# Kernel tuning notes

Hardware: AMD Instinct MI355X
Metric: run time of the kernel (lower is better)

The kernel has to match this reference:

```python
import jax, jax.numpy as jnp
import numpy as np
from jax import lax

N, C, H, W = 5, 256, 128, 128
RATIO = 16
KS = 3
SIGMA = 1.0
THRE = 0.01


def _conv2d_same(x, w):
    k = w.shape[-1]
    p = (k - 1) // 2
    return lax.conv_general_dilated(x, w, (1, 1), [(p, p), (p, p)],
                                    dimension_numbers=('NCHW', 'OIHW', 'NCHW'))


def _gaussian2d():
    c = KS // 2
    x, y = np.mgrid[-c:KS - c, -c:KS - c]
    g = 1.0 / (2.0 * np.pi * SIGMA) * np.exp(-(x ** 2 + y ** 2) / (2.0 * SIGMA ** 2))
    return jnp.asarray(g, jnp.float32).reshape(1, 1, KS, KS)


def _gaussian1d():
    x = np.arange(-(KS - 1) // 2, (KS + 1) // 2, dtype=np.float32)
    g = np.exp(-x ** 2 / (2.0 * SIGMA ** 2))
    g = g / g.sum()
    return jnp.asarray(g, jnp.float32).reshape(1, 1, KS)


def setup_inputs() -> dict:
    key = jax.random.key(0)
    ks = jax.random.split(key, 12)
    s = 0.05
    return {
        'feat': jax.random.normal(ks[0], (N, C, H, W), jnp.float32),
        'mlp_w1': jax.random.normal(ks[1], (C // RATIO, C), jnp.float32) * s,
        'mlp_w2': jax.random.normal(ks[2], (C, C // RATIO), jnp.float32) * s,
        'sp_req_w': jax.random.normal(ks[3], (1, 2, 3, 3), jnp.float32) * s,
        'ch_fus_w': jax.random.normal(ks[4], (C, 2 * C), jnp.float32) * s,
        'sp_fus_w': jax.random.normal(ks[5], (1, 2), jnp.float32) * s,
        'st_w1': jax.random.normal(ks[6], (4 * C, 2 * C), jnp.float32) * s,
        'st_b1': jax.random.normal(ks[7], (4 * C,), jnp.float32) * s,
        'st_w2': jax.random.normal(ks[8], (4 * C, 4 * C), jnp.float32) * s,
        'st_b2': jax.random.normal(ks[9], (4 * C,), jnp.float32) * s,
        'st_w3': jax.random.normal(ks[10], (1, 4 * C), jnp.float32) * s,
        'st_b3': jax.random.normal(ks[11], (1,), jnp.float32) * s,
    }


def _forward(feat, mlp_w1, mlp_w2, sp_req_w, ch_fus_w, sp_fus_w,
             st_w1, st_b1, st_w2, st_b2, st_w3, st_b3):
    g2 = _gaussian2d()
    g1 = _gaussian1d()

    # Channel_Request_Attention: shared MLP on avg- and max-pooled features
    avg = feat.mean(axis=(2, 3))          # [N, C]
    mx = feat.max(axis=(2, 3))            # [N, C]
    mlp = lambda v: jax.nn.relu(v @ mlp_w1.T) @ mlp_w2.T
    ch_att = jax.nn.sigmoid(mlp(avg) + mlp(mx))  # [N, C]

    # Spatial_Request_Attention: 3x3 conv over [mean, max] channel stats
    sp_in = jnp.concatenate([feat.mean(axis=1, keepdims=True),
                             feat.max(axis=1, keepdims=True)], axis=1)  # [N,2,H,W]
    sp_att = jax.nn.sigmoid(_conv2d_same(sp_in, sp_req_w))  # [N,1,H,W]

    # gaussian-smoothed activation map
    act = _conv2d_same(jax.nn.sigmoid(feat.mean(axis=1, keepdims=True)), g2)  # [N,1,H,W]

    ego_ch = 1.0 - ch_att[0]   # [C]
    ego_sp = 1.0 - sp_att[0]   # [1,H,W]

    # channel_fusion: 1x1 conv on concat([ego_request, collaborator_att]) -> split weight
    Wa, Wb = ch_fus_w[:, :C], ch_fus_w[:, C:]
    ch_coef = jax.nn.sigmoid(ego_ch @ Wa.T + ch_att[1:] @ Wb.T)  # [N-1, C]
    # smooth over the channel axis with 1D gaussian
    ch_coef = lax.conv_general_dilated(ch_coef[:, None, :], g1, (1,), [(KS // 2, KS // 2)],
                                       dimension_numbers=('NCH', 'OIH', 'NCH'))[:, 0, :]

    # spatial_fusion: 1x1 conv on concat([ego_sp_request, collaborator_sp_att])
    wa, wb = sp_fus_w[0, 0], sp_fus_w[0, 1]
    sp_coef = jax.nn.sigmoid(wa * ego_sp[None] + wb * sp_att[1:])  # [N-1,1,H,W]
    sp_coef = _conv2d_same(sp_coef, g2)

    sparse_matrix = ch_coef[:, :, None, None] * sp_coef * act[1:]  # [N-1,C,H,W]
    mask = (sparse_matrix > THRE).astype(feat.dtype)
    mean_rate = mask.mean()  # equal-sized per-collaborator means -> global mean

    sparse_feature = jnp.concatenate([feat[:1], feat[1:] * mask], axis=0)  # [N,C,H,W]
    sparse_mask = jnp.concatenate([jnp.ones_like(feat[:1]), mask], axis=0)

    def stat(x):
        h = jax.nn.relu(jnp.einsum('nchw,oc->nohw', x, st_w1) + st_b1[None, :, None, None])
        h = jax.nn.relu(jnp.einsum('nchw,oc->nohw', h, st_w2) + st_b2[None, :, None, None])
        return jnp.einsum('nchw,oc->nohw', h, st_w3) + st_b3[None, :, None, None]

    T = stat(jnp.concatenate([feat, sparse_feature], axis=1))
    feat_prime = jnp.roll(feat, -1, axis=0)
    T_prime = stat(jnp.concatenate([feat_prime, sparse_feature], axis=1))

    joint = (-jax.nn.softplus(-T)).mean()
    marginal = jax.nn.softplus(T_prime).mean()
    total_loss = -(joint - marginal)

    return sparse_feature, total_loss, mean_rate, sparse_mask


def reference(feat, mlp_w1, mlp_w2, sp_req_w, ch_fus_w, sp_fus_w,
              st_w1, st_b1, st_w2, st_b2, st_w3, st_b3):
    return _forward(feat, mlp_w1, mlp_w2, sp_req_w, ch_fus_w, sp_fus_w,
                    st_w1, st_b1, st_w2, st_b2, st_w3, st_b3)
```

## Files before the change

kernel.cpp:

```cpp
#include <hip/hip_runtime.h>
#include <cmath>

#define NIMG 5
#define CCH  256
#define HHH  128
#define WWW  128
#define HW   16384
#define NPIX 81920
#define SF_ELEMS 20971520
#define LOSS_OFF 20971520
#define RATE_OFF 20971521
#define MASK_OFF 20971522

typedef __attribute__((ext_vector_type(4))) float f32x4;
typedef __attribute__((ext_vector_type(8))) __bf16 bf16x8;
typedef __attribute__((ext_vector_type(8))) unsigned short u16x8;

__device__ __forceinline__ unsigned short f32_to_bf16(float f) {
  unsigned int u = __float_as_uint(f);
  u += 0x7FFFu + ((u >> 16) & 1u);
  return (unsigned short)(u >> 16);
}

__device__ __forceinline__ double sigmoid_d(double x) { return 1.0 / (1.0 + exp(-x)); }

__device__ __forceinline__ float softplus_f(float x) {
  if (x > 20.f) return x;
  if (x < -20.f) return expf(x);
  return log1pf(expf(x));
}

__device__ __forceinline__ double g2w(int ky, int kx) {
  int d2 = (ky - 1) * (ky - 1) + (kx - 1) * (kx - 1);
  double g = 0.15915494309189535 * exp(-0.5 * (double)d2);
  return (double)(float)g;
}

__device__ __forceinline__ void gload16(const unsigned short* g, void* l) {
  __builtin_amdgcn_global_load_lds((const __attribute__((address_space(1))) void*)g,
                                   (__attribute__((address_space(3))) void*)l, 16, 0, 0);
}

__global__ void k0_init(double* S1, double* S2, unsigned long long* cnt) {
  if (threadIdx.x == 0 && blockIdx.x == 0) { *S1 = 0.0; *S2 = 0.0; *cnt = 0ull; }
}

__global__ void k1_rednc(const float* __restrict__ feat, double* __restrict__ avg_d,
                         double* __restrict__ mx_d) {
  int nc = blockIdx.x;
  int t = threadIdx.x;
  const float* p = feat + (size_t)nc * HW;
  double s = 0.0;
  float m = -3.4e38f;
  for (int i = t; i < HW; i += 256) { float v = p[i]; s += (double)v; m = fmaxf(m, v); }
  __shared__ double sd[256];
  __shared__ float sm[256];
  sd[t] = s; sm[t] = m;
  __syncthreads();
  for (int o = 128; o > 0; o >>= 1) {
    if (t < o) { sd[t] += sd[t + o]; sm[t] = fmaxf(sm[t], sm[t + o]); }
    __syncthreads();
  }
  if (t == 0) { avg_d[nc] = sd[0] / 16384.0; mx_d[nc] = (double)sm[0]; }
}

__global__ void k2_rednp(const float* __restrict__ feat, double* __restrict__ chmean,
                         double* __restrict__ chmax) {
  int gid = blockIdx.x * 256 + threadIdx.x;
  int n = gid >> 14, p = gid & (HW - 1);
  const float* base = feat + (size_t)n * CCH * HW + p;
  double s = 0.0;
  float m = -3.4e38f;
  for (int c = 0; c < CCH; ++c) { float v = base[(size_t)c * HW]; s += (double)v; m = fmaxf(m, v); }
  chmean[gid] = s / 256.0;
  chmax[gid] = (double)m;
}

__global__ void k3_chan(const double* __restrict__ avg_d, const double* __restrict__ mx_d,
                        const float* __restrict__ w1, const float* __restrict__ w2,
                        const float* __restrict__ fus, double* __restrict__ chcoef_d) {
  __shared__ double hid_a[NIMG][16], hid_m[NIMG][16];
  __shared__ double att[NIMG][CCH];
  __shared__ double sig[4][CCH];
  int t = threadIdx.x;
  if (t < NIMG * 16) {
    int n = t / 16, j = t % 16;
    double sa = 0.0, sx = 0.0;
    for (int c = 0; c < CCH; ++c) {
      double w = (double)w1[j * CCH + c];
      sa += avg_d[n * CCH + c] * w;
      sx += mx_d[n * CCH + c] * w;
    }
    hid_a[n][j] = sa > 0.0 ? sa : 0.0;
    hid_m[n][j] = sx > 0.0 ? sx : 0.0;
  }
  __syncthreads();
  for (int n = 0; n < NIMG; ++n) {
    double oa = 0.0, om = 0.0;
    for (int j = 0; j < 16; ++j) {
      double w = (double)w2[t * 16 + j];
      oa += hid_a[n][j] * w;
      om += hid_m[n][j] * w;
    }
    att[n][t] = sigmoid_d(oa + om);
  }
  __syncthreads();
  for (int m = 0; m < 4; ++m) {
    double s = 0.0;
    for (int k = 0; k < CCH; ++k) {
      s += (1.0 - att[0][k]) * (double)fus[t * 512 + k]
         + att[m + 1][k] * (double)fus[t * 512 + 256 + k];
    }
    sig[m][t] = sigmoid_d(s);
  }
  __syncthreads();
  float a32 = (float)exp(-0.5);
  float s32 = (a32 + 1.0f) + a32;
  double ge = (double)(a32 / s32);
  double gc = (double)(1.0f / s32);
  for (int m = 0; m < 4; ++m) {
    double L = (t > 0) ? sig[m][t - 1] : 0.0;
    double R = (t < 255) ? sig[m][t + 1] : 0.0;
    chcoef_d[m * CCH + t] = ge * L + gc * sig[m][t] + ge * R;
  }
}

__global__ void k4_spatial(const double* __restrict__ chmean, const double* __restrict__ chmax,
                           const float* __restrict__ spw, double* __restrict__ spatt,
                           double* __restrict__ actb) {
  int gid = blockIdx.x * 256 + threadIdx.x;
  int n = gid >> 14, p = gid & (HW - 1);
  int y = p >> 7, x = p & 127;
  const double* cm = chmean + (size_t)n * HW;
  const double* cx = chmax + (size_t)n * HW;
  double s = 0.0, a = 0.0;
  for (int ky = 0; ky < 3; ++ky) {
    int yy = y + ky - 1;
    if ((unsigned)yy >= 128u) continue;
    for (int kx = 0; kx < 3; ++kx) {
      int xx = x + kx - 1;
      if ((unsigned)xx >= 128u) continue;
      int q = (yy << 7) + xx;
      s += (double)spw[ky * 3 + kx] * cm[q] + (double)spw[9 + ky * 3 + kx] * cx[q];
      a += g2w(ky, kx) * sigmoid_d(cm[q]);
    }
  }
  spatt[gid] = sigmoid_d(s);
  actb[gid] = a;
}

__global__ void k5a_spsig(const double* __restrict__ spatt, const float* __restrict__ fus2,
                          double* __restrict__ spsig) {
  int gid = blockIdx.x * 256 + threadIdx.x;
  int m = gid >> 14, p = gid & (HW - 1);
  double wa = (double)fus2[0], wb = (double)fus2[1];
  double ego = 1.0 - spatt[p];
  spsig[gid] = sigmoid_d(wa * ego + wb * spatt[(size_t)(m + 1) * HW + p]);
}

__global__ void k5b_spcoef(const double* __restrict__ spsig, const double* __restrict__ actb,
                           double* __restrict__ spact) {
  int gid = blockIdx.x * 256 + threadIdx.x;
  int m = gid >> 14, p = gid & (HW - 1);
  int y = p >> 7, x = p & 127;
  const double* sp = spsig + (size_t)m * HW;
  double s = 0.0;
  for (int ky = 0; ky < 3; ++ky) {
    int yy = y + ky - 1;
    if ((unsigned)yy >= 128u) continue;
    for (int kx = 0; kx < 3; ++kx) {
      int xx = x + kx - 1;
      if ((unsigned)xx >= 128u) continue;
      s += g2w(ky, kx) * sp[(yy << 7) + xx];
    }
  }
  spact[gid] = s * actb[(size_t)(m + 1) * HW + p];
}

__global__ void k6_mask(const float* __restrict__ feat, const double* __restrict__ chcoef,
                        const double* __restrict__ spact, float* __restrict__ out_sf,
                        float* __restrict__ out_mask, unsigned long long* __restrict__ cnt) {
  const int nth = gridDim.x * blockDim.x;
  int cl = 0;
  for (int g4 = blockIdx.x * blockDim.x + threadIdx.x; g4 < SF_ELEMS / 4; g4 += nth) {
    size_t e = (size_t)g4 * 4;
    int nc = (int)(e >> 14);
    int p = (int)(e & (HW - 1));
    int n = nc >> 8, c = nc & 255;
    f32x4 v = *(const f32x4*)&feat[e];
    f32x4 mk;
    if (n == 0) {
      mk = (f32x4){1.f, 1.f, 1.f, 1.f};
    } else {
      double cc = chcoef[(n - 1) * CCH + c];
      const double* sp = &spact[(size_t)(n - 1) * HW + p];
#pragma unroll
      for (int l = 0; l < 4; ++l) {
        float m = (cc * sp[l] > 0.01) ? 1.f : 0.f;
        mk[l] = m;
        cl += (m != 0.f);
      }
    }
    f32x4 o;
#pragma unroll
    for (int l = 0; l < 4; ++l) o[l] = v[l] * mk[l];
    __builtin_nontemporal_store(o, (f32x4*)&out_sf[e]);
    __builtin_nontemporal_store(mk, (f32x4*)&out_mask[e]);
  }
#pragma unroll
  for (int off = 32; off > 0; off >>= 1) cl += __shfl_down(cl, off);
  if ((threadIdx.x & 63) == 0 && cl > 0) atomicAdd(cnt, (unsigned long long)cl);
}

__global__ void k7_wconv(const float* __restrict__ w1, const float* __restrict__ w2,
                         unsigned short* __restrict__ W1b, unsigned short* __restrict__ W2b) {
  int gid = blockIdx.x * 256 + threadIdx.x;
  if (gid < 524288) W1b[gid] = f32_to_bf16(w1[gid]);
  W2b[gid] = f32_to_bf16(w2[gid]);
}

__global__ void k6b_transpose(const float* __restrict__ feat, const float* __restrict__ sf,
                              unsigned short* __restrict__ featT, unsigned short* __restrict__ sfT) {
  __shared__ unsigned short tf[64][65];
  __shared__ unsigned short tsb[64][65];
  const int bid = blockIdx.x;
  const int n  = bid >> 10;
  const int r  = bid & 1023;
  const int ct = r >> 8;
  const int pt = r & 255;
  const int c0 = ct << 6, p0 = pt << 6;
  const int t = threadIdx.x;
  {
    const int cy = t >> 2, px4 = (t & 3) << 4;
    const float* fp = feat + ((size_t)n * 256 + c0 + cy) * HW + p0 + px4;
    const float* sp = sf   + ((size_t)n * 256 + c0 + cy) * HW + p0 + px4;
#pragma unroll
    for (int i = 0; i < 4; ++i) {
      f32x4 v = *(const f32x4*)(fp + i * 4);
      f32x4 u = *(const f32x4*)(sp + i * 4);
#pragma unroll
      for (int j = 0; j < 4; ++j) {
        tf[cy][px4 + i * 4 + j]  = f32_to_bf16(v[j]);
        tsb[cy][px4 + i * 4 + j] = f32_to_bf16(u[j]);
      }
    }
  }
  __syncthreads();
  {
    const int py = t >> 2, cx = (t & 3) << 4;
    u16x8 o0, o1, q0, q1;
#pragma unroll
    for (int k = 0; k < 8; ++k) { o0[k] = tf[cx + k][py];     q0[k] = tsb[cx + k][py]; }
#pragma unroll
    for (int k = 0; k < 8; ++k) { o1[k] = tf[cx + 8 + k][py]; q1[k] = tsb[cx + 8 + k][py]; }
    size_t ob = ((size_t)n * HW + p0 + py) * 256 + c0 + cx;
    *(u16x8*)&featT[ob]     = o0;
    *(u16x8*)&featT[ob + 8] = o1;
    *(u16x8*)&sfT[ob]       = q0;
    *(u16x8*)&sfT[ob + 8]   = q1;
  }
}

__global__ void kT0_zero(float* __restrict__ T) {
  int g = blockIdx.x * 256 + threadIdx.x;
  for (int i = g; i < 163840; i += gridDim.x * 256) T[i] = 0.f;
}

template<int NT, bool L1>
__global__ __launch_bounds__(256, 4) void k8_gemm(
    const unsigned short* __restrict__ A0,
    const unsigned short* __restrict__ A1,
    const unsigned short* __restrict__ Wb,
    const float* __restrict__ bias,
    const float* __restrict__ w3,
    unsigned short* __restrict__ H1,
    float* __restrict__ Tout,
    int m_base) {
  __shared__ unsigned short lds[16384];

  const int bid0 = blockIdx.x;
  const int cpx = gridDim.x >> 3;
  const int sb = (bid0 & 7) * cpx + (bid0 >> 3);
  const int mt = sb >> 3, nt = sb & 7;

  const int t = threadIdx.x, l = t & 63, w = t >> 6;
  const int wr = w >> 1, wc = w & 1;
  const int n16 = l & 15, quad = l >> 4;
  constexpr int ldb = L1 ? 512 : 1024;

  const unsigned short* base_feat = nullptr;
  const unsigned short* base_sf = nullptr;
  const unsigned short* base_a = nullptr;
  if constexpr (L1) {
    const int g0 = m_base + mt * 128;
    const int branch = (g0 >= NPIX) ? 1 : 0;
    const int rl = g0 - branch * NPIX;
    const int img = rl >> 14;
    const int p0 = rl & (HW - 1);
    const int img_f = branch ? (img + 1 == NIMG ? 0 : img + 1) : img;
    base_feat = A0 + ((size_t)img_f * HW + p0) * 256;
    base_sf   = A1 + ((size_t)img   * HW + p0) * 256;
  } else {
    base_a = A0 + (size_t)(mt * 128) * 1024;
  }
  const unsigned short* base_b = Wb + (size_t)(nt * 128) * ldb;

  const int r0 = l >> 2;
  const int kk = (l & 3) * 8;

  auto stage = [&](int buf, int ts) {
    const unsigned short* Ap;
    size_t as;
    if constexpr (L1) {
      if (ts < 8) { Ap = base_feat + ts * 32; } else { Ap = base_sf + (ts - 8) * 32; }
      as = 256;
    } else {
      Ap = base_a + ts * 32;
      as = 1024;
    }
    const unsigned short* Bp = base_b + ts * 32;
#pragma unroll
    for (int j = 0; j < 2; ++j) {
      const int s = w * 2 + j;
      gload16(Ap + (size_t)(s * 16 + r0) * as + kk, (void*)&lds[buf * 4096 + s * 512]);
      gload16(Bp + (size_t)(s * 16 + r0) * (size_t)ldb + kk, (void*)&lds[8192 + buf * 4096 + s * 512]);
    }
  };

  f32x4 acc[4][4];
  {
    f32x4 z = {0.f, 0.f, 0.f, 0.f};
#pragma unroll
    for (int g = 0; g < 4; ++g)
#pragma unroll
      for (int j = 0; j < 4; ++j) acc[g][j] = z;
  }

  stage(0, 0);
  for (int ts = 0; ts < NT; ++ts) {
    const int cur = ts & 1;
    if (ts + 1 < NT) {
      stage(cur ^ 1, ts + 1);
      asm volatile("s_waitcnt vmcnt(4)" ::: "memory");
    } else {
      asm volatile("s_waitcnt vmcnt(0)" ::: "memory");
    }
    asm volatile("s_barrier" ::: "memory");

    const int abase = cur * 4096 + (wr * 64) * 32;
    const int bbase = 8192 + cur * 4096 + (wc * 64) * 32;
    bf16x8 af[4], bg[4];
#pragma unroll
    for (int g = 0; g < 4; ++g) af[g] = *(const bf16x8*)&lds[abase + (g * 16 + n16) * 32 + quad * 8];
#pragma unroll
    for (int j = 0; j < 4; ++j) bg[j] = *(const bf16x8*)&lds[bbase + (j * 16 + n16) * 32 + quad * 8];
#pragma unroll
    for (int g = 0; g < 4; ++g)
#pragma unroll
      for (int j = 0; j < 4; ++j)
        acc[g][j] = __builtin_amdgcn_mfma_f32_16x16x32_bf16(af[g], bg[j], acc[g][j], 0, 0, 0);

    asm volatile("s_waitcnt lgkmcnt(0)" ::: "memory");
    asm volatile("s_barrier" ::: "memory");
  }

  const int colb = nt * 128 + wc * 64;
  if constexpr (L1) {
    const size_t mloc0 = (size_t)(mt * 128 + wr * 64);
#pragma unroll
    for (int j = 0; j < 4; ++j) {
      const int col = colb + j * 16 + n16;
      const float bv = bias[col];
#pragma unroll
      for (int g = 0; g < 4; ++g) {
#pragma unroll
        for (int rr = 0; rr < 4; ++rr) {
          float v = acc[g][j][rr] + bv;
          v = v > 0.f ? v : 0.f;
          H1[(mloc0 + g * 16 + quad * 4 + rr) * 1024 + col] = f32_to_bf16(v);
        }
      }
    }
  } else {
    float rs[4][4];
#pragma unroll
    for (int g = 0; g < 4; ++g)
#pragma unroll
      for (int rr = 0; rr < 4; ++rr) rs[g][rr] = 0.f;
#pragma unroll
    for (int j = 0; j < 4; ++j) {
      const int col = colb + j * 16 + n16;
      const float bv = bias[col];
      const float wv = w3[col];
#pragma unroll
      for (int g = 0; g < 4; ++g) {
#pragma unroll
        for (int rr = 0; rr < 4; ++rr) {
          float v = acc[g][j][rr] + bv;
          v = v > 0.f ? v : 0.f;
          rs[g][rr] += v * wv;
        }
      }
    }
#pragma unroll
    for (int off = 1; off < 16; off <<= 1) {
#pragma unroll
      for (int g = 0; g < 4; ++g)
#pragma unroll
        for (int rr = 0; rr < 4; ++rr) rs[g][rr] += __shfl_xor(rs[g][rr], off);
    }
    if (n16 == 0) {
      const int row0 = m_base + mt * 128 + wr * 64;
#pragma unroll
      for (int g = 0; g < 4; ++g)
#pragma unroll
        for (int rr = 0; rr < 4; ++rr)
          atomicAdd(&Tout[row0 + g * 16 + quad * 4 + rr], rs[g][rr]);
    }
  }
}

__global__ void k8c_red(const float* __restrict__ T, const float* __restrict__ b3,
                        double* __restrict__ S1, double* __restrict__ S2) {
  const int gid = blockIdx.x * 256 + threadIdx.x;
  const int stride = gridDim.x * 256;
  const float bv = b3[0];
  double s1 = 0.0, s2 = 0.0;
  for (int r = gid; r < 163840; r += stride) {
    float Tv = T[r] + bv;
    if (r < NPIX) s1 += (double)softplus_f(-Tv);
    else          s2 += (double)softplus_f(Tv);
  }
#pragma unroll
  for (int off = 32; off > 0; off >>= 1) {
    s1 += __shfl_down(s1, off);
    s2 += __shfl_down(s2, off);
  }
  __shared__ double l1[4], l2[4];
  const int wv = threadIdx.x >> 6;
  if ((threadIdx.x & 63) == 0) { l1[wv] = s1; l2[wv] = s2; }
  __syncthreads();
  if (threadIdx.x == 0) {
    atomicAdd(S1, l1[0] + l1[1] + l1[2] + l1[3]);
    atomicAdd(S2, l2[0] + l2[1] + l2[2] + l2[3]);
  }
}

__device__ __forceinline__ int xidx(int row, int c) {
  return row * 512 + ((((c >> 3) ^ (row & 7)) << 3) | (c & 7));
}
__device__ __forceinline__ int hidx(int row, int oc) {
  return 32768 + row * 256 + ((((oc >> 3) ^ (row & 7)) << 3) | (oc & 7));
}

__global__ __launch_bounds__(1024, 4) void k8_stat(
    const float* __restrict__ feat, const float* __restrict__ sf,
    const unsigned short* __restrict__ W1b, const unsigned short* __restrict__ W2b,
    const float* __restrict__ b1, const float* __restrict__ b2,
    const float* __restrict__ w3, const float* __restrict__ b3,
    double* __restrict__ S1, double* __restrict__ S2) {
  __shared__ unsigned short lds[49280];
  float* t_acc = (float*)&lds[49152];

  const int bid = blockIdx.x;
  const int n = bid >> 9;
  const int p0 = (bid & 511) << 5;
  const int n1 = (n + 1 == NIMG) ? 0 : n + 1;

  const int t = threadIdx.x;
  const int lane = t & 63;
  const int w = t >> 6;
  const int n16 = lane & 15;
  const int quad = lane >> 4;

  {
    const int c = t & 511;
    const int half = t >> 9;
    if (t < 64) t_acc[t] = 0.f;
#pragma unroll
    for (int rb = 0; rb < 2; ++rb) {
      const float* s = (c < 256)
          ? feat + ((size_t)(rb ? n1 : n) * CCH + c) * HW + p0
          : sf + ((size_t)n * CCH + (c - 256)) * HW + p0;
      const f32x4* s4 = (const f32x4*)(s + half * 16);
#pragma unroll
      for (int i = 0; i < 4; ++i) {
        f32x4 v = __builtin_nontemporal_load(s4 + i);
        const int prow = rb * 32 + half * 16 + i * 4;
#pragma unroll
        for (int l = 0; l < 4; ++l) lds[xidx(prow + l, c)] = f32_to_bf16(v[l]);
      }
    }
  }
  __syncthreads();

  f32x4 acc2[4][4];
  {
    f32x4 z = {0.f, 0.f, 0.f, 0.f};
#pragma unroll
    for (int g = 0; g < 4; ++g)
#pragma unroll
      for (int jt = 0; jt < 4; ++jt) acc2[g][jt] = z;
  }

  for (int nc = 0; nc < 4; ++nc) {
    f32x4 acc1[4];
    {
      f32x4 z = {0.f, 0.f, 0.f, 0.f};
#pragma unroll
      for (int g = 0; g < 4; ++g) acc1[g] = z;
    }
    const int o = nc * 256 + w * 16 + n16;
    const unsigned short* Wrow = W1b + (size_t)o * 512;
    bf16x8 bnxt = *(const bf16x8*)&Wrow[quad * 8];
    for (int ks = 0; ks < 16; ++ks) {
      bf16x8 b = bnxt;
      if (ks < 15) bnxt = *(const bf16x8*)&Wrow[(ks + 1) * 32 + quad * 8];
      const int cb = ks * 32 + quad * 8;
#pragma unroll
      for (int g = 0; g < 4; ++g) {
        bf16x8 a = *(const bf16x8*)&lds[xidx(g * 16 + n16, cb)];
        acc1[g] = __builtin_amdgcn_mfma_f32_16x16x32_bf16(a, b, acc1[g], 0, 0, 0);
      }
    }
    __syncthreads();

    {
      const float bv = b1[o];
      const int ol = w * 16 + n16;
#pragma unroll
      for (int g = 0; g < 4; ++g) {
#pragma unroll
        for (int r = 0; r < 4; ++r) {
          const int row = g * 16 + quad * 4 + r;
          float v = acc1[g][r] + bv;
          v = v > 0.f ? v : 0.f;
          lds[hidx(row, ol)] = f32_to_bf16(v);
        }
      }
    }
    __syncthreads();

    for (int ksl = 0; ksl < 8; ++ksl) {
      const int ocb = ksl * 32 + quad * 8;
      bf16x8 a[4];
#pragma unroll
      for (int g = 0; g < 4; ++g) a[g] = *(const bf16x8*)&lds[hidx(g * 16 + n16, ocb)];
#pragma unroll
      for (int jt = 0; jt < 4; ++jt) {
        const int o2 = w * 64 + jt * 16 + n16;
        bf16x8 b = *(const bf16x8*)&W2b[(size_t)o2 * 1024 + nc * 256 + ocb];
#pragma unroll
        for (int g = 0; g < 4; ++g)
          acc2[g][jt] = __builtin_amdgcn_mfma_f32_16x16x32_bf16(a[g], b, acc2[g][jt], 0, 0, 0);
      }
    }
  }

  float tp[4][4];
#pragma unroll
  for (int g = 0; g < 4; ++g)
#pragma unroll
    for (int r = 0; r < 4; ++r) tp[g][r] = 0.f;
#pragma unroll
  for (int jt = 0; jt < 4; ++jt) {
    const int o2 = w * 64 + jt * 16 + n16;
    const float bv = b2[o2];
    const float wv = w3[o2];
#pragma unroll
    for (int g = 0; g < 4; ++g) {
#pragma unroll
      for (int r = 0; r < 4; ++r) {
        float v = acc2[g][jt][r] + bv;
        v = v > 0.f ? v : 0.f;
        tp[g][r] += v * wv;
      }
    }
  }
#pragma unroll
  for (int off = 1; off < 16; off <<= 1) {
#pragma unroll
    for (int g = 0; g < 4; ++g)
#pragma unroll
      for (int r = 0; r < 4; ++r) tp[g][r] += __shfl_xor(tp[g][r], off);
  }
  if (n16 == 0) {
#pragma unroll
    for (int g = 0; g < 4; ++g)
#pragma unroll
      for (int r = 0; r < 4; ++r) atomicAdd(&t_acc[g * 16 + quad * 4 + r], tp[g][r]);
  }
  __syncthreads();

  if (t < 64) {
    const float T = t_acc[t] + b3[0];
    float v = (t < 32) ? softplus_f(-T) : softplus_f(T);
#pragma unroll
    for (int off = 16; off > 0; off >>= 1) v += __shfl_down(v, off);
    if (t == 0) atomicAdd(S1, (double)v);
    if (t == 32) atomicAdd(S2, (double)v);
  }
}

__global__ void k9_final(const double* __restrict__ S1, const double* __restrict__ S2,
                         const unsigned long long* __restrict__ cnt, float* __restrict__ out) {
  if (threadIdx.x == 0 && blockIdx.x == 0) {
    out[LOSS_OFF] = (float)(((*S1) + (*S2)) / 81920.0);
    out[RATE_OFF] = (float)((double)(*cnt) / 16777216.0);
  }
}

#define WS_FEATT 8388608ull
#define WS_SFT   50331648ull
#define WS_H1    92274688ull
#define WS_T     176160768ull
#define WS_NEED  176816128ull

extern "C" void kernel_launch(void* const* d_in, const int* in_sizes, int n_in,
                              void* d_out, int out_size, void* d_ws, size_t ws_size,
                              hipStream_t stream) {
  const float* feat     = (const float*)d_in[0];
  const float* mlp_w1   = (const float*)d_in[1];
  const float* mlp_w2   = (const float*)d_in[2];
  const float* sp_req_w = (const float*)d_in[3];
  const float* ch_fus_w = (const float*)d_in[4];
  const float* sp_fus_w = (const float*)d_in[5];
  const float* st_w1    = (const float*)d_in[6];
  const float* st_b1    = (const float*)d_in[7];
  const float* st_w2    = (const float*)d_in[8];
  const float* st_b2    = (const float*)d_in[9];
  const float* st_w3    = (const float*)d_in[10];
  const float* st_b3    = (const float*)d_in[11];
  float* out = (float*)d_out;

  char* ws = (char*)d_ws;
  double* S1     = (double*)(ws + 0);
  double* S2     = (double*)(ws + 8);
  unsigned long long* cnt = (unsigned long long*)(ws + 16);
  double* avg_d  = (double*)(ws + 64);
  double* mx_d   = (double*)(ws + 10304);
  double* chmean = (double*)(ws + 20544);
  double* chmax  = (double*)(ws + 675904);
  double* spatt  = (double*)(ws + 1331264);
  double* actb   = (double*)(ws + 1986624);
  double* chcoef = (double*)(ws + 2652224);
  double* spsig  = (double*)(ws + 2660416);
  double* spact  = (double*)(ws + 3184704);
  unsigned short* W1b = (unsigned short*)(ws + 3708992);
  unsigned short* W2b = (unsigned short*)(ws + 4757568);

  k0_init<<<1, 64, 0, stream>>>(S1, S2, cnt);
  k1_rednc<<<1280, 256, 0, stream>>>(feat, avg_d, mx_d);
  k2_rednp<<<320, 256, 0, stream>>>(feat, chmean, chmax);
  k3_chan<<<1, 256, 0, stream>>>(avg_d, mx_d, mlp_w1, mlp_w2, ch_fus_w, chcoef);
  k4_spatial<<<320, 256, 0, stream>>>(chmean, chmax, sp_req_w, spatt, actb);
  k5a_spsig<<<256, 256, 0, stream>>>(spatt, sp_fus_w, spsig);
  k5b_spcoef<<<256, 256, 0, stream>>>(spsig, actb, spact);
  k7_wconv<<<4096, 256, 0, stream>>>(st_w1, st_w2, W1b, W2b);
  k6_mask<<<2048, 256, 0, stream>>>(feat, chcoef, spact, out, out + MASK_OFF, cnt);

  if (ws_size >= WS_NEED) {
    unsigned short* featT = (unsigned short*)(ws + WS_FEATT);
    unsigned short* sfT   = (unsigned short*)(ws + WS_SFT);
    unsigned short* H1    = (unsigned short*)(ws + WS_H1);
    float* Tb             = (float*)(ws + WS_T);
    kT0_zero<<<160, 256, 0, stream>>>(Tb);
    k6b_transpose<<<5120, 256, 0, stream>>>(feat, out, featT, sfT);
    for (int c = 0; c < 5; ++c) {
      k8_gemm<16, true><<<2048, 256, 0, stream>>>(featT, sfT, W1b, st_b1, nullptr, H1, nullptr, c * 32768);
      k8_gemm<32, false><<<2048, 256, 0, stream>>>(H1, nullptr, W2b, st_b2, st_w3, nullptr, Tb, c * 32768);
    }
    k8c_red<<<160, 256, 0, stream>>>(Tb, st_b3, S1, S2);
  } else {
    k8_stat<<<2560, 1024, 0, stream>>>(feat, out, W1b, W2b, st_b1, st_b2, st_w3, st_b3, S1, S2);
  }

  k9_final<<<1, 64, 0, stream>>>(S1, S2, cnt, out);
}
```

Baseline: 1.229 ms.

## Share sparse-feature half of first stat GEMM between joint and marginal branches

The first-layer GEMM now processes one image at a time and computes the sparse-feature half of the K dimension once. It then forks the accumulator into the joint branch (feat[n]) and the marginal branch (feat[n+1]) instead of recomputing it for each. This removes about a quarter of the layer-1 MFMA work and A-tile loads, at the cost of doubled accumulator registers, so launch bounds drop to 2 blocks per CU. It also adds a nontemporal load in the mask kernel and reorders the zero and transpose launches.

```diff
diff --git a/kernel.cpp b/kernel.cpp
--- a/kernel.cpp
+++ b/kernel.cpp
@@ -187,7 +187,7 @@
     int nc = (int)(e >> 14);
     int p = (int)(e & (HW - 1));
     int n = nc >> 8, c = nc & 255;
-    f32x4 v = *(const f32x4*)&feat[e];
+    f32x4 v = __builtin_nontemporal_load((const f32x4*)&feat[e]);
     f32x4 mk;
     if (n == 0) {
       mk = (f32x4){1.f, 1.f, 1.f, 1.f};
@@ -266,16 +266,10 @@
   for (int i = g; i < 163840; i += gridDim.x * 256) T[i] = 0.f;
 }
 
-template<int NT, bool L1>
-__global__ __launch_bounds__(256, 4) void k8_gemm(
-    const unsigned short* __restrict__ A0,
-    const unsigned short* __restrict__ A1,
-    const unsigned short* __restrict__ Wb,
-    const float* __restrict__ bias,
-    const float* __restrict__ w3,
-    unsigned short* __restrict__ H1,
-    float* __restrict__ Tout,
-    int m_base) {
+__global__ __launch_bounds__(256, 2) void k8_gemm1p(
+    const unsigned short* __restrict__ featT, const unsigned short* __restrict__ sfT,
+    const unsigned short* __restrict__ W1b, const float* __restrict__ b1,
+    unsigned short* __restrict__ H1img, int n) {
   __shared__ unsigned short lds[16384];
 
   const int bid0 = blockIdx.x;
@@ -286,44 +280,124 @@
   const int t = threadIdx.x, l = t & 63, w = t >> 6;
   const int wr = w >> 1, wc = w & 1;
   const int n16 = l & 15, quad = l >> 4;
-  constexpr int ldb = L1 ? 512 : 1024;
-
-  const unsigned short* base_feat = nullptr;
-  const unsigned short* base_sf = nullptr;
-  const unsigned short* base_a = nullptr;
-  if constexpr (L1) {
-    const int g0 = m_base + mt * 128;
-    const int branch = (g0 >= NPIX) ? 1 : 0;
-    const int rl = g0 - branch * NPIX;
-    const int img = rl >> 14;
-    const int p0 = rl & (HW - 1);
-    const int img_f = branch ? (img + 1 == NIMG ? 0 : img + 1) : img;
-    base_feat = A0 + ((size_t)img_f * HW + p0) * 256;
-    base_sf   = A1 + ((size_t)img   * HW + p0) * 256;
-  } else {
-    base_a = A0 + (size_t)(mt * 128) * 1024;
-  }
-  const unsigned short* base_b = Wb + (size_t)(nt * 128) * ldb;
+  const int n1 = (n + 1 == NIMG) ? 0 : n + 1;
+
+  const unsigned short* baseS  = sfT   + ((size_t)n  * HW + mt * 128) * 256;
+  const unsigned short* baseF  = featT + ((size_t)n  * HW + mt * 128) * 256;
+  const unsigned short* baseF1 = featT + ((size_t)n1 * HW + mt * 128) * 256;
+  const unsigned short* baseB  = W1b + (size_t)(nt * 128) * 512;
 
   const int r0 = l >> 2;
   const int kk = (l & 3) * 8;
 
-  auto stage = [&](int buf, int ts) {
+  auto stage = [&](int buf, int u) {
     const unsigned short* Ap;
-    size_t as;
-    if constexpr (L1) {
-      if (ts < 8) { Ap = base_feat + ts * 32; } else { Ap = base_sf + (ts - 8) * 32; }
-      as = 256;
-    } else {
-      Ap = base_a + ts * 32;
-      as = 1024;
-    }
-    const unsigned short* Bp = base_b + ts * 32;
+    int kb;
+    if (u < 8)       { Ap = baseS  + u * 32;        kb = 256 + u * 32; }
+    else if (u < 16) { Ap = baseF  + (u - 8) * 32;  kb = (u - 8) * 32;  }
+    else             { Ap = baseF1 + (u - 16) * 32; kb = (u - 16) * 32; }
+    const unsigned short* Bp = baseB + kb;
 #pragma unroll
     for (int j = 0; j < 2; ++j) {
       const int s = w * 2 + j;
-      gload16(Ap + (size_t)(s * 16 + r0) * as + kk, (void*)&lds[buf * 4096 + s * 512]);
-      gload16(Bp + (size_t)(s * 16 + r0) * (size_t)ldb + kk, (void*)&lds[8192 + buf * 4096 + s * 512]);
+      gload16(Ap + (size_t)(s * 16 + r0) * 256 + kk, (void*)&lds[buf * 4096 + s * 512]);
+      gload16(Bp + (size_t)(s * 16 + r0) * 512 + kk, (void*)&lds[8192 + buf * 4096 + s * 512]);
+    }
+  };
+
+  f32x4 accJ[4][4], accM[4][4];
+  {
+    f32x4 z = {0.f, 0.f, 0.f, 0.f};
+#pragma unroll
+    for (int g = 0; g < 4; ++g)
+#pragma unroll
+      for (int j = 0; j < 4; ++j) accJ[g][j] = z;
+  }
+
+  auto kstep = [&](f32x4 (&acc)[4][4], int u, bool last) {
+    const int cur = u & 1;
+    if (!last) {
+      stage(cur ^ 1, u + 1);
+      asm volatile("s_waitcnt vmcnt(4)" ::: "memory");
+    } else {
+      asm volatile("s_waitcnt vmcnt(0)" ::: "memory");
+    }
+    asm volatile("s_barrier" ::: "memory");
+    const int abase = cur * 4096 + (wr * 64) * 32;
+    const int bbase = 8192 + cur * 4096 + (wc * 64) * 32;
+    bf16x8 af[4], bg[4];
+#pragma unroll
+    for (int g = 0; g < 4; ++g) af[g] = *(const bf16x8*)&lds[abase + (g * 16 + n16) * 32 + quad * 8];
+#pragma unroll
+    for (int j = 0; j < 4; ++j) bg[j] = *(const bf16x8*)&lds[bbase + (j * 16 + n16) * 32 + quad * 8];
+#pragma unroll
+    for (int g = 0; g < 4; ++g)
+#pragma unroll
+      for (int j = 0; j < 4; ++j)
+        acc[g][j] = __builtin_amdgcn_mfma_f32_16x16x32_bf16(af[g], bg[j], acc[g][j], 0, 0, 0);
+    asm volatile("s_waitcnt lgkmcnt(0)" ::: "memory");
+    asm volatile("s_barrier" ::: "memory");
+  };
+
+  stage(0, 0);
+  for (int u = 0; u < 8; ++u) kstep(accJ, u, false);
+#pragma unroll
+  for (int g = 0; g < 4; ++g)
+#pragma unroll
+    for (int j = 0; j < 4; ++j) accM[g][j] = accJ[g][j];
+  for (int u = 8; u < 16; ++u) kstep(accJ, u, false);
+  for (int u = 16; u < 24; ++u) kstep(accM, u, u == 23);
+
+  const int colb = nt * 128 + wc * 64;
+#pragma unroll
+  for (int j = 0; j < 4; ++j) {
+    const int col = colb + j * 16 + n16;
+    const float bv = b1[col];
+#pragma unroll
+    for (int g = 0; g < 4; ++g) {
+#pragma unroll
+      for (int rr = 0; rr < 4; ++rr) {
+        const size_t row = (size_t)(mt * 128 + wr * 64 + g * 16 + quad * 4 + rr);
+        float vj = accJ[g][j][rr] + bv;
+        vj = vj > 0.f ? vj : 0.f;
+        H1img[row * 1024 + col] = f32_to_bf16(vj);
+        float vm = accM[g][j][rr] + bv;
+        vm = vm > 0.f ? vm : 0.f;
+        H1img[(row + 16384) * 1024 + col] = f32_to_bf16(vm);
+      }
+    }
+  }
+}
+
+__global__ __launch_bounds__(256, 2) void k8_gemm2(
+    const unsigned short* __restrict__ H1img, const unsigned short* __restrict__ W2b,
+    const float* __restrict__ b2, const float* __restrict__ w3,
+    float* __restrict__ Tout, int n) {
+  __shared__ unsigned short lds[16384];
+
+  const int bid0 = blockIdx.x;
+  const int cpx = gridDim.x >> 3;
+  const int sb = (bid0 & 7) * cpx + (bid0 >> 3);
+  const int mt = sb >> 3, nt = sb & 7;
+
+  const int t = threadIdx.x, l = t & 63, w = t >> 6;
+  const int wr = w >> 1, wc = w & 1;
+  const int n16 = l & 15, quad = l >> 4;
+
+  const unsigned short* base_a = H1img + (size_t)(mt * 128) * 1024;
+  const unsigned short* base_b = W2b + (size_t)(nt * 128) * 1024;
+
+  const int r0 = l >> 2;
+  const int kk = (l & 3) * 8;
+
+  auto stage = [&](int buf, int ts) {
+    const unsigned short* Ap = base_a + ts * 32;
+    const unsigned short* Bp = base_b + ts * 32;
+#pragma unroll
+    for (int j = 0; j < 2; ++j) {
+      const int s = w * 2 + j;
+      gload16(Ap + (size_t)(s * 16 + r0) * 1024 + kk, (void*)&lds[buf * 4096 + s * 512]);
+      gload16(Bp + (size_t)(s * 16 + r0) * 1024 + kk, (void*)&lds[8192 + buf * 4096 + s * 512]);
     }
   };
 
@@ -337,9 +411,9 @@
   }
 
   stage(0, 0);
-  for (int ts = 0; ts < NT; ++ts) {
+  for (int ts = 0; ts < 32; ++ts) {
     const int cur = ts & 1;
-    if (ts + 1 < NT) {
+    if (ts + 1 < 32) {
       stage(cur ^ 1, ts + 1);
       asm volatile("s_waitcnt vmcnt(4)" ::: "memory");
     } else {
@@ -365,58 +439,40 @@
   }
 
   const int colb = nt * 128 + wc * 64;
-  if constexpr (L1) {
-    const size_t mloc0 = (size_t)(mt * 128 + wr * 64);
-#pragma unroll
-    for (int j = 0; j < 4; ++j) {
-      const int col = colb + j * 16 + n16;
-      const float bv = bias[col];
-#pragma unroll
-      for (int g = 0; g < 4; ++g) {
-#pragma unroll
-        for (int rr = 0; rr < 4; ++rr) {
-          float v = acc[g][j][rr] + bv;
-          v = v > 0.f ? v : 0.f;
-          H1[(mloc0 + g * 16 + quad * 4 + rr) * 1024 + col] = f32_to_bf16(v);
-        }
-      }
-    }
-  } else {
-    float rs[4][4];
-#pragma unroll
-    for (int g = 0; g < 4; ++g)
-#pragma unroll
-      for (int rr = 0; rr < 4; ++rr) rs[g][rr] = 0.f;
-#pragma unroll
-    for (int j = 0; j < 4; ++j) {
-      const int col = colb + j * 16 + n16;
-      const float bv = bias[col];
-      const float wv = w3[col];
-#pragma unroll
-      for (int g = 0; g < 4; ++g) {
-#pragma unroll
-        for (int rr = 0; rr < 4; ++rr) {
-          float v = acc[g][j][rr] + bv;
-          v = v > 0.f ? v : 0.f;
-          rs[g][rr] += v * wv;
-        }
-      }
-    }
-#pragma unroll
-    for (int off = 1; off < 16; off <<= 1) {
-#pragma unroll
-      for (int g = 0; g < 4; ++g)
-#pragma unroll
-        for (int rr = 0; rr < 4; ++rr) rs[g][rr] += __shfl_xor(rs[g][rr], off);
-    }
-    if (n16 == 0) {
-      const int row0 = m_base + mt * 128 + wr * 64;
-#pragma unroll
-      for (int g = 0; g < 4; ++g)
-#pragma unroll
-        for (int rr = 0; rr < 4; ++rr)
-          atomicAdd(&Tout[row0 + g * 16 + quad * 4 + rr], rs[g][rr]);
-    }
+  float rs[4][4];
+#pragma unroll
+  for (int g = 0; g < 4; ++g)
+#pragma unroll
+    for (int rr = 0; rr < 4; ++rr) rs[g][rr] = 0.f;
+#pragma unroll
+  for (int j = 0; j < 4; ++j) {
+    const int col = colb + j * 16 + n16;
+    const float bv = b2[col];
+    const float wv = w3[col];
+#pragma unroll
+    for (int g = 0; g < 4; ++g) {
+#pragma unroll
+      for (int rr = 0; rr < 4; ++rr) {
+        float v = acc[g][j][rr] + bv;
+        v = v > 0.f ? v : 0.f;
+        rs[g][rr] += v * wv;
+      }
+    }
+  }
+#pragma unroll
+  for (int off = 1; off < 16; off <<= 1) {
+#pragma unroll
+    for (int g = 0; g < 4; ++g)
+#pragma unroll
+      for (int rr = 0; rr < 4; ++rr) rs[g][rr] += __shfl_xor(rs[g][rr], off);
+  }
+  if (n16 == 0) {
+    const int rbase = (mt < 128) ? (n * HW + mt * 128) : (NPIX + n * HW + (mt - 128) * 128);
+#pragma unroll
+    for (int g = 0; g < 4; ++g)
+#pragma unroll
+      for (int rr = 0; rr < 4; ++rr)
+        atomicAdd(&Tout[rbase + wr * 64 + g * 16 + quad * 4 + rr], rs[g][rr]);
   }
 }
 
@@ -662,13 +718,13 @@
   if (ws_size >= WS_NEED) {
     unsigned short* featT = (unsigned short*)(ws + WS_FEATT);
     unsigned short* sfT   = (unsigned short*)(ws + WS_SFT);
-    unsigned short* H1    = (unsigned short*)(ws + WS_H1);
+    unsigned short* H1img = (unsigned short*)(ws + WS_H1);
     float* Tb             = (float*)(ws + WS_T);
+    k6b_transpose<<<5120, 256, 0, stream>>>(feat, out, featT, sfT);
     kT0_zero<<<160, 256, 0, stream>>>(Tb);
-    k6b_transpose<<<5120, 256, 0, stream>>>(feat, out, featT, sfT);
-    for (int c = 0; c < 5; ++c) {
-      k8_gemm<16, true><<<2048, 256, 0, stream>>>(featT, sfT, W1b, st_b1, nullptr, H1, nullptr, c * 32768);
-      k8_gemm<32, false><<<2048, 256, 0, stream>>>(H1, nullptr, W2b, st_b2, st_w3, nullptr, Tb, c * 32768);
+    for (int n = 0; n < NIMG; ++n) {
+      k8_gemm1p<<<1024, 256, 0, stream>>>(featT, sfT, W1b, st_b1, H1img, n);
+      k8_gemm2<<<2048, 256, 0, stream>>>(H1img, W2b, st_b2, st_w3, Tb, n);
     }
     k8c_red<<<160, 256, 0, stream>>>(Tb, st_b3, S1, S2);
   } else {
```

After: 1.177 ms. -4.2%, faster.
